# Optimization experiments

Hardware: AMD Instinct MI355X
Metric: run time of the kernel (lower is better)

## Reference

```python
import jax, jax.numpy as jnp
import numpy as np

BN_EPS = 1e-5


def setup_inputs() -> dict:
    key = jax.random.key(0)
    ks = jax.random.split(key, 6)
    B, C, H, W, Lt, Hd = 4, 256, 64, 64, 4096, 128
    w_scale = 1.0 / np.sqrt(C)
    return {
        "input_i": jax.random.normal(ks[0], (B, C, H, W), jnp.float32),
        "input_t": jax.random.normal(ks[1], (B, C, Lt), jnp.float32),
        "w_img_q": jax.random.normal(ks[2], (Hd, C), jnp.float32) * w_scale,
        "bnq_gamma": jnp.ones((Hd,), jnp.float32),
        "bnq_beta": jnp.zeros((Hd,), jnp.float32),
        "bnq_mean": jnp.zeros((Hd,), jnp.float32),
        "bnq_var": jnp.ones((Hd,), jnp.float32),
        "w_img_k": jax.random.normal(ks[3], (Hd, C), jnp.float32) * w_scale,
        "bnk_gamma": jnp.ones((Hd,), jnp.float32),
        "bnk_beta": jnp.zeros((Hd,), jnp.float32),
        "bnk_mean": jnp.zeros((Hd,), jnp.float32),
        "bnk_var": jnp.ones((Hd,), jnp.float32),
        "w_text_k": jax.random.normal(ks[4], (Hd, C), jnp.float32) * w_scale,
        "b_text_k": jnp.zeros((Hd,), jnp.float32),
        "w_text_q": jax.random.normal(ks[5], (Hd, C), jnp.float32) * w_scale,
        "b_text_q": jnp.zeros((Hd,), jnp.float32),
    }


def _conv1x1_bn(x, w, gamma, beta, mean, var):
    # x: [B,C,H,W], w: [O,C] -> [B,O,H,W], then eval-mode BatchNorm2d
    y = jnp.einsum('bchw,oc->bohw', x, w)
    s = (gamma / jnp.sqrt(var + BN_EPS))[None, :, None, None]
    return (y - mean[None, :, None, None]) * s + beta[None, :, None, None]


def reference(input_i, input_t, w_img_q, bnq_gamma, bnq_beta, bnq_mean, bnq_var,
              w_img_k, bnk_gamma, bnk_beta, bnk_mean, bnk_var,
              w_text_k, b_text_k, w_text_q, b_text_q):
    B, C, H, W = input_i.shape
    Hd = w_img_q.shape[0]
    inv_scale = jnp.asarray(Hd, input_i.dtype) ** 0.5  # module divides by hid_dim**-0.5

    # Image -> text attention
    i_q = _conv1x1_bn(input_i, w_img_q, bnq_gamma, bnq_beta, bnq_mean, bnq_var)
    i_q = i_q.reshape(B, Hd, -1).transpose(0, 2, 1)          # [B, Ni, Hd]
    t_flat = input_t.reshape(B, C, -1).transpose(0, 2, 1)    # [B, Lt, C]
    t_k = t_flat @ w_text_k.T + b_text_k                     # [B, Lt, Hd]
    iscores = jnp.einsum('bnd,bmd->bnm', i_q, t_k) * inv_scale
    att_i = jax.nn.softmax(iscores, axis=-1)
    output_i = jnp.einsum('bnm,bmc->bnc', att_i, t_flat)     # [B, Ni, C]

    # Text -> image attention (the permute/reshape/permute chain is identity)
    t_q = t_flat @ w_text_q.T + b_text_q                     # [B, Lt, Hd]
    i_k = _conv1x1_bn(input_i, w_img_k, bnk_gamma, bnk_beta, bnk_mean, bnk_var)
    i_k = i_k.reshape(B, Hd, -1).transpose(0, 2, 1)          # [B, Ni, Hd]
    i_v = input_i.reshape(B, C, -1).transpose(0, 2, 1)       # [B, Ni, C]
    tscores = jnp.einsum('bmd,bnd->bmn', t_q, i_k) * inv_scale
    att_t = jax.nn.softmax(tscores, axis=-1)
    output_t = jnp.einsum('bmn,bnc->bmc', att_t, i_v)        # [B, Lt, C]

    return (output_i, output_t)
```

## Files before the change

### kernel.cpp

```cpp
#include <hip/hip_runtime.h>
#include <hip/hip_bf16.h>
#include <math.h>
#include <stdint.h>

#define B_  4
#define C_  256
#define N_  4096
#define HD_ 128

typedef __attribute__((ext_vector_type(8))) short bf16x8;
typedef __attribute__((ext_vector_type(4))) float f32x4;
typedef __attribute__((ext_vector_type(4))) int   i32x4;

#define WF_SHORTS   ((size_t)4*8*8*2*512)
#define PROJ_SHORTS ((size_t)4*256*4*2*512)
#define VT_SHORTS   ((size_t)4*128*16*512)

static __device__ __forceinline__ short f2bf(float x){
  union { float f; unsigned u; } v; v.f = x;
  unsigned r = v.u + 0x7fffu + ((v.u >> 16) & 1u);
  return (short)(r >> 16);
}
static __device__ __forceinline__ float bf2f(short h){
  union { unsigned u; float f; } v; v.u = ((unsigned)(unsigned short)h) << 16;
  return v.f;
}

__global__ void wfrag_kernel(const float* __restrict__ w0, const float* __restrict__ w1,
                             const float* __restrict__ w2, const float* __restrict__ w3,
                             short* __restrict__ wf)
{
  int job = blockIdx.x, dt = blockIdx.y, ck = blockIdx.z;
  const float* W = job==0 ? w0 : (job==1 ? w1 : (job==2 ? w2 : w3));
  int l = threadIdx.x, g = l>>4, ln = l&15;
  bf16x8 hi, lo;
#pragma unroll
  for (int j=0;j<8;j++){
    int d = dt*16 + ln;
    int c = ck*32 + 4*g + (j&3) + 16*(j>>2);
    float x = W[d*C_ + c];
    short h = f2bf(x);
    hi[j] = h;
    lo[j] = f2bf(x - bf2f(h));
  }
  size_t base = (((size_t)(job*8+dt)*8 + ck)*2)*512 + (size_t)l*8;
  *reinterpret_cast<bf16x8*>(wf + base)       = hi;
  *reinterpret_cast<bf16x8*>(wf + base + 512) = lo;
}

__global__ __launch_bounds__(256,2) void proj_kernel(
    const float* __restrict__ Xi, const float* __restrict__ Xt,
    const short* __restrict__ wf,
    const float* __restrict__ bnq_g, const float* __restrict__ bnq_b,
    const float* __restrict__ bnq_m, const float* __restrict__ bnq_v,
    const float* __restrict__ bnk_g, const float* __restrict__ bnk_b,
    const float* __restrict__ bnk_m, const float* __restrict__ bnk_v,
    const float* __restrict__ btk, const float* __restrict__ btq,
    short* __restrict__ proj)
{
  const int job = blockIdx.z, b = blockIdx.y;
  const int tid = threadIdx.x, wid = tid>>6, l = tid&63, g = l>>4, ln = l&15;
  const float* X = (job==0 || job==3) ? Xi : Xt;
  const int n0 = blockIdx.x*256 + wid*64;

  const f32x4 fzero = {0.f,0.f,0.f,0.f};
  f32x4 acc[4][8];
#pragma unroll
  for (int nt=0;nt<4;nt++)
#pragma unroll
    for (int dt=0;dt<8;dt++) acc[nt][dt] = fzero;

#pragma unroll 1
  for (int ck=0; ck<8; ck++){
    bf16x8 Bh[4], Bl[4];
#pragma unroll
    for (int nt=0;nt<4;nt++){
#pragma unroll
      for (int j=0;j<8;j++){
        int c = ck*32 + 4*g + (j&3) + 16*(j>>2);
        int n = n0 + nt*16 + ln;
        float x = X[((size_t)b*C_ + c)*N_ + n];
        short h = f2bf(x);
        Bh[nt][j] = h;
        Bl[nt][j] = f2bf(x - bf2f(h));
      }
    }
#pragma unroll
    for (int dt=0;dt<8;dt++){
      const short* af = wf + (((size_t)(job*8+dt)*8 + ck)*2)*512 + (size_t)l*8;
      bf16x8 Ah = *reinterpret_cast<const bf16x8*>(af);
      bf16x8 Al = *reinterpret_cast<const bf16x8*>(af + 512);
#pragma unroll
      for (int nt=0;nt<4;nt++){
        acc[nt][dt] = __builtin_amdgcn_mfma_f32_16x16x32_bf16(Ah, Bh[nt], acc[nt][dt], 0,0,0);
        acc[nt][dt] = __builtin_amdgcn_mfma_f32_16x16x32_bf16(Ah, Bl[nt], acc[nt][dt], 0,0,0);
        acc[nt][dt] = __builtin_amdgcn_mfma_f32_16x16x32_bf16(Al, Bh[nt], acc[nt][dt], 0,0,0);
      }
    }
  }

#pragma unroll
  for (int nt=0;nt<4;nt++){
    int tglob = (n0>>4) + nt;
#pragma unroll
    for (int kc=0;kc<4;kc++){
      bf16x8 hi, lo;
#pragma unroll
      for (int j=0;j<8;j++){
        int dt = 2*kc + (j>>2), r = j&3;
        int d = dt*16 + 4*g + r;
        float y = acc[nt][dt][r];
        float s, t;
        if (job==0){ s = bnq_g[d]*rsqrtf(bnq_v[d]+1e-5f); t = bnq_b[d]-bnq_m[d]*s; }
        else if (job==3){ s = bnk_g[d]*rsqrtf(bnk_v[d]+1e-5f); t = bnk_b[d]-bnk_m[d]*s; }
        else if (job==1){ s = 1.f; t = btk[d]; }
        else            { s = 1.f; t = btq[d]; }
        y = y*s + t;
        short h = f2bf(y);
        hi[j] = h;
        lo[j] = f2bf(y - bf2f(h));
      }
      short* dst = proj + (size_t)job*PROJ_SHORTS
                 + ((((size_t)b*256 + tglob)*4 + kc)*2)*512 + (size_t)l*8;
      *reinterpret_cast<bf16x8*>(dst)       = hi;
      *reinterpret_cast<bf16x8*>(dst + 512) = lo;
    }
  }
}

__global__ __launch_bounds__(512,1) void vtile_kernel(
    const float* __restrict__ Xi, const float* __restrict__ Xt,
    short* __restrict__ vt)
{
  int kt = blockIdx.x, b = blockIdx.y, dir = blockIdx.z;
  const float* X = (dir==0) ? Xt : Xi;
  __shared__ float tile[256*33];
  int tid = threadIdx.x;
#pragma unroll
  for (int i=0;i<16;i++){
    int idx = tid + i*512, row = idx>>5, col = idx&31;
    tile[row*33+col] = X[((size_t)b*C_ + row)*N_ + (size_t)kt*32 + col];
  }
  __syncthreads();
  int wid = tid>>6, l = tid&63, g = l>>4, ln = l&15;
#pragma unroll
  for (int w2=0;w2<2;w2++){
    int cc = wid*2 + w2;
    bf16x8 o;
#pragma unroll
    for (int j=0;j<8;j++){
      int c = cc*16 + ln;
      int col = 4*g + (j&3) + 16*(j>>2);
      o[j] = f2bf(tile[c*33 + col]);
    }
    *reinterpret_cast<bf16x8*>(vt + (size_t)dir*VT_SHORTS
        + (((size_t)b*128 + kt)*16 + cc)*512 + (size_t)l*8) = o;
  }
}

__global__ __launch_bounds__(512,2) void flash_kernel(
    const short* __restrict__ proj, const short* __restrict__ vt,
    float* __restrict__ outp)
{
  const int qb = blockIdx.x, b = blockIdx.y, dir = blockIdx.z;
  const short* Qt = proj + (size_t)(2*dir)*PROJ_SHORTS;
  const short* Kt = proj + (size_t)(2*dir+1)*PROJ_SHORTS;
  const short* Vt = vt + (size_t)dir*VT_SHORTS;
  float* Od = outp + (size_t)dir*((size_t)B_*N_*C_);

  __shared__ short lds[2*16384];

  const int tid = threadIdx.x, wid = tid>>6, l = tid&63, g = l>>4, ln = l&15;

  const int tq = qb*8 + wid;
  bf16x8 qf[4][2];
#pragma unroll
  for (int kc=0;kc<4;kc++)
#pragma unroll
    for (int h=0;h<2;h++)
      qf[kc][h] = *reinterpret_cast<const bf16x8*>(
        Qt + ((((size_t)b*256 + tq)*4 + kc)*2 + h)*512 + (size_t)l*8);

  const f32x4 fzero = {0.f,0.f,0.f,0.f};
  f32x4 oacc[16];
#pragma unroll
  for (int cc=0;cc<16;cc++) oacc[cc] = fzero;
  float mrun = -INFINITY, lrun = 0.f;
  const float SCALE = 11.313708498984761f;

  {
    const i32x4* ks = reinterpret_cast<const i32x4*>(Kt + ((size_t)(b*256))*4096) + tid*2;
    const i32x4* vs = reinterpret_cast<const i32x4*>(Vt + ((size_t)(b*128))*8192) + tid*2;
    i32x4 a0=ks[0], a1=ks[1], a2=vs[0], a3=vs[1];
    i32x4* lk = reinterpret_cast<i32x4*>(lds) + tid*2;
    i32x4* lv = reinterpret_cast<i32x4*>(lds + 8192) + tid*2;
    lk[0]=a0; lk[1]=a1; lv[0]=a2; lv[1]=a3;
  }
  __syncthreads();

#pragma unroll 1
  for (int s=0; s<128; s++){
    const int cur = s & 1;
    i32x4 st0, st1, st2, st3;
    if (s < 127){
      const i32x4* ks = reinterpret_cast<const i32x4*>(Kt + ((size_t)(b*256 + 2*(s+1)))*4096) + tid*2;
      const i32x4* vs = reinterpret_cast<const i32x4*>(Vt + ((size_t)(b*128 + (s+1)))*8192) + tid*2;
      st0=ks[0]; st1=ks[1]; st2=vs[0]; st3=vs[1];
    }
    const short* lk = lds + cur*16384;
    const short* lv = lk + 8192;

    f32x4 sacc[2];
    sacc[0] = fzero; sacc[1] = fzero;
#pragma unroll
    for (int kvt=0;kvt<2;kvt++){
#pragma unroll
      for (int kc=0;kc<4;kc++){
        bf16x8 kh  = *reinterpret_cast<const bf16x8*>(lk + (size_t)(kvt*8 + kc*2 + 0)*512 + l*8);
        bf16x8 klo = *reinterpret_cast<const bf16x8*>(lk + (size_t)(kvt*8 + kc*2 + 1)*512 + l*8);
        sacc[kvt] = __builtin_amdgcn_mfma_f32_16x16x32_bf16(kh,  qf[kc][0], sacc[kvt], 0,0,0);
        sacc[kvt] = __builtin_amdgcn_mfma_f32_16x16x32_bf16(kh,  qf[kc][1], sacc[kvt], 0,0,0);
        sacc[kvt] = __builtin_amdgcn_mfma_f32_16x16x32_bf16(klo, qf[kc][0], sacc[kvt], 0,0,0);
      }
    }

    float sv[8];
#pragma unroll
    for (int kvt=0;kvt<2;kvt++)
#pragma unroll
      for (int r=0;r<4;r++) sv[kvt*4+r] = sacc[kvt][r]*SCALE;
    float tmax = sv[0];
#pragma unroll
    for (int i=1;i<8;i++) tmax = fmaxf(tmax, sv[i]);
    tmax = fmaxf(tmax, __shfl_xor(tmax, 16));
    tmax = fmaxf(tmax, __shfl_xor(tmax, 32));
    float mnew  = fmaxf(mrun, tmax);
    float alpha = __expf(mrun - mnew);
    float p[8], psum = 0.f;
#pragma unroll
    for (int i=0;i<8;i++){ p[i] = __expf(sv[i]-mnew); psum += p[i]; }
    psum += __shfl_xor(psum, 16);
    psum += __shfl_xor(psum, 32);
    lrun = lrun*alpha + psum;
    mrun = mnew;

    bf16x8 pa;
#pragma unroll
    for (int i=0;i<8;i++) pa[i] = f2bf(p[i]);
#pragma unroll
    for (int cc=0;cc<16;cc++) oacc[cc] *= alpha;

#pragma unroll
    for (int cc=0;cc<16;cc++){
      bf16x8 vf = *reinterpret_cast<const bf16x8*>(lv + (size_t)cc*512 + l*8);
      oacc[cc] = __builtin_amdgcn_mfma_f32_16x16x32_bf16(vf, pa, oacc[cc], 0,0,0);
    }

    if (s < 127){
      const int nxt = cur^1;
      i32x4* lkw = reinterpret_cast<i32x4*>(lds + nxt*16384) + tid*2;
      i32x4* lvw = reinterpret_cast<i32x4*>(lds + nxt*16384 + 8192) + tid*2;
      lkw[0]=st0; lkw[1]=st1; lvw[0]=st2; lvw[1]=st3;
    }
    __syncthreads();
  }

  float inv = 1.f / lrun;
  int qrow = qb*128 + wid*16 + ln;
  float* orow = Od + ((size_t)b*N_ + qrow)*C_;
#pragma unroll
  for (int cc=0;cc<16;cc++){
    f32x4 o = oacc[cc]*inv;
    *reinterpret_cast<f32x4*>(orow + cc*16 + 4*g) = o;
  }
}

extern "C" void kernel_launch(void* const* d_in, const int* in_sizes, int n_in,
                              void* d_out, int out_size, void* d_ws, size_t ws_size,
                              hipStream_t stream)
{
  (void)in_sizes; (void)n_in; (void)out_size; (void)ws_size;
  const float* input_i = (const float*)d_in[0];
  const float* input_t = (const float*)d_in[1];
  const float* w_img_q = (const float*)d_in[2];
  const float* bnq_g   = (const float*)d_in[3];
  const float* bnq_b   = (const float*)d_in[4];
  const float* bnq_m   = (const float*)d_in[5];
  const float* bnq_v   = (const float*)d_in[6];
  const float* w_img_k = (const float*)d_in[7];
  const float* bnk_g   = (const float*)d_in[8];
  const float* bnk_b   = (const float*)d_in[9];
  const float* bnk_m   = (const float*)d_in[10];
  const float* bnk_v   = (const float*)d_in[11];
  const float* w_text_k = (const float*)d_in[12];
  const float* b_text_k = (const float*)d_in[13];
  const float* w_text_q = (const float*)d_in[14];
  const float* b_text_q = (const float*)d_in[15];

  short* ws   = (short*)d_ws;
  short* wf   = ws;
  short* proj = ws + WF_SHORTS;
  short* vt   = ws + WF_SHORTS + 4*PROJ_SHORTS;

  wfrag_kernel<<<dim3(4,8,8), 64, 0, stream>>>(w_img_q, w_text_k, w_text_q, w_img_k, wf);
  proj_kernel<<<dim3(16,4,4), 256, 0, stream>>>(input_i, input_t, wf,
      bnq_g, bnq_b, bnq_m, bnq_v, bnk_g, bnk_b, bnk_m, bnk_v,
      b_text_k, b_text_q, proj);
  vtile_kernel<<<dim3(128,4,2), 512, 0, stream>>>(input_i, input_t, vt);
  flash_kernel<<<dim3(32,4,2), 512, 0, stream>>>(proj, vt, (float*)d_out);
}
```

Before: 272.5 us.

## Process two query tiles per wave, fold scale into Q, lazy softmax rescale

Each wave now handles two 16-row query tiles, halving the block to 256 threads, so every K and V fragment read from LDS feeds twice as many MFMAs. The softmax scale is folded into the Q projection epilogue, which removes a per-score multiply in the flash loop. The running max is only updated, and the accumulators rescaled, when the new tile max exceeds the old one by more than 8. This trades higher register pressure and fewer waves per CU for less LDS traffic and less per-iteration softmax work.

```diff
diff --git a/kernel.cpp b/kernel.cpp
--- a/kernel.cpp
+++ b/kernel.cpp
@@ -62,6 +62,7 @@
   const int tid = threadIdx.x, wid = tid>>6, l = tid&63, g = l>>4, ln = l&15;
   const float* X = (job==0 || job==3) ? Xi : Xt;
   const int n0 = blockIdx.x*256 + wid*64;
+  const float SCALE = 11.313708498984761f;
 
   const f32x4 fzero = {0.f,0.f,0.f,0.f};
   f32x4 acc[4][8];
@@ -111,10 +112,11 @@
         int d = dt*16 + 4*g + r;
         float y = acc[nt][dt][r];
         float s, t;
-        if (job==0){ s = bnq_g[d]*rsqrtf(bnq_v[d]+1e-5f); t = bnq_b[d]-bnq_m[d]*s; }
+        if (job==0){ s = bnq_g[d]*rsqrtf(bnq_v[d]+1e-5f); t = bnq_b[d]-bnq_m[d]*s;
+                     s *= SCALE; t *= SCALE; }
         else if (job==3){ s = bnk_g[d]*rsqrtf(bnk_v[d]+1e-5f); t = bnk_b[d]-bnk_m[d]*s; }
         else if (job==1){ s = 1.f; t = btk[d]; }
-        else            { s = 1.f; t = btq[d]; }
+        else            { s = SCALE; t = btq[d]*SCALE; }
         y = y*s + t;
         short h = f2bf(y);
         hi[j] = h;
@@ -158,7 +160,7 @@
   }
 }
 
-__global__ __launch_bounds__(512,2) void flash_kernel(
+__global__ __launch_bounds__(256,1) void flash_kernel(
     const short* __restrict__ proj, const short* __restrict__ vt,
     float* __restrict__ outp)
 {
@@ -172,106 +174,132 @@
 
   const int tid = threadIdx.x, wid = tid>>6, l = tid&63, g = l>>4, ln = l&15;
 
-  const int tq = qb*8 + wid;
-  bf16x8 qf[4][2];
-#pragma unroll
-  for (int kc=0;kc<4;kc++)
-#pragma unroll
-    for (int h=0;h<2;h++)
-      qf[kc][h] = *reinterpret_cast<const bf16x8*>(
-        Qt + ((((size_t)b*256 + tq)*4 + kc)*2 + h)*512 + (size_t)l*8);
+  bf16x8 qf[2][4][2];
+#pragma unroll
+  for (int qt=0;qt<2;qt++){
+    const int tq = qb*8 + wid*2 + qt;
+#pragma unroll
+    for (int kc=0;kc<4;kc++)
+#pragma unroll
+      for (int h=0;h<2;h++)
+        qf[qt][kc][h] = *reinterpret_cast<const bf16x8*>(
+          Qt + ((((size_t)b*256 + tq)*4 + kc)*2 + h)*512 + (size_t)l*8);
+  }
 
   const f32x4 fzero = {0.f,0.f,0.f,0.f};
-  f32x4 oacc[16];
-#pragma unroll
-  for (int cc=0;cc<16;cc++) oacc[cc] = fzero;
-  float mrun = -INFINITY, lrun = 0.f;
-  const float SCALE = 11.313708498984761f;
+  f32x4 oacc[2][16];
+#pragma unroll
+  for (int qt=0;qt<2;qt++)
+#pragma unroll
+    for (int cc=0;cc<16;cc++) oacc[qt][cc] = fzero;
+  float mrun[2] = {-INFINITY, -INFINITY};
+  float lrun[2] = {0.f, 0.f};
 
   {
-    const i32x4* ks = reinterpret_cast<const i32x4*>(Kt + ((size_t)(b*256))*4096) + tid*2;
-    const i32x4* vs = reinterpret_cast<const i32x4*>(Vt + ((size_t)(b*128))*8192) + tid*2;
-    i32x4 a0=ks[0], a1=ks[1], a2=vs[0], a3=vs[1];
-    i32x4* lk = reinterpret_cast<i32x4*>(lds) + tid*2;
-    i32x4* lv = reinterpret_cast<i32x4*>(lds + 8192) + tid*2;
-    lk[0]=a0; lk[1]=a1; lv[0]=a2; lv[1]=a3;
+    const i32x4* gk = reinterpret_cast<const i32x4*>(Kt + ((size_t)(b*256))*4096);
+    const i32x4* gv = reinterpret_cast<const i32x4*>(Vt + ((size_t)(b*128))*8192);
+    i32x4* lkw = reinterpret_cast<i32x4*>(lds);
+    i32x4* lvw = reinterpret_cast<i32x4*>(lds + 8192);
+#pragma unroll
+    for (int i=0;i<4;i++){
+      lkw[tid + 256*i] = gk[tid + 256*i];
+      lvw[tid + 256*i] = gv[tid + 256*i];
+    }
   }
   __syncthreads();
 
 #pragma unroll 1
   for (int s=0; s<128; s++){
     const int cur = s & 1;
-    i32x4 st0, st1, st2, st3;
+    i32x4 kst[4], vst[4];
     if (s < 127){
-      const i32x4* ks = reinterpret_cast<const i32x4*>(Kt + ((size_t)(b*256 + 2*(s+1)))*4096) + tid*2;
-      const i32x4* vs = reinterpret_cast<const i32x4*>(Vt + ((size_t)(b*128 + (s+1)))*8192) + tid*2;
-      st0=ks[0]; st1=ks[1]; st2=vs[0]; st3=vs[1];
+      const i32x4* gk = reinterpret_cast<const i32x4*>(Kt + ((size_t)(b*256 + 2*(s+1)))*4096);
+      const i32x4* gv = reinterpret_cast<const i32x4*>(Vt + ((size_t)(b*128 + (s+1)))*8192);
+#pragma unroll
+      for (int i=0;i<4;i++){ kst[i] = gk[tid + 256*i]; vst[i] = gv[tid + 256*i]; }
     }
     const short* lk = lds + cur*16384;
     const short* lv = lk + 8192;
 
-    f32x4 sacc[2];
-    sacc[0] = fzero; sacc[1] = fzero;
+    f32x4 sacc[2][2];
+    sacc[0][0]=fzero; sacc[0][1]=fzero; sacc[1][0]=fzero; sacc[1][1]=fzero;
 #pragma unroll
     for (int kvt=0;kvt<2;kvt++){
 #pragma unroll
       for (int kc=0;kc<4;kc++){
         bf16x8 kh  = *reinterpret_cast<const bf16x8*>(lk + (size_t)(kvt*8 + kc*2 + 0)*512 + l*8);
         bf16x8 klo = *reinterpret_cast<const bf16x8*>(lk + (size_t)(kvt*8 + kc*2 + 1)*512 + l*8);
-        sacc[kvt] = __builtin_amdgcn_mfma_f32_16x16x32_bf16(kh,  qf[kc][0], sacc[kvt], 0,0,0);
-        sacc[kvt] = __builtin_amdgcn_mfma_f32_16x16x32_bf16(kh,  qf[kc][1], sacc[kvt], 0,0,0);
-        sacc[kvt] = __builtin_amdgcn_mfma_f32_16x16x32_bf16(klo, qf[kc][0], sacc[kvt], 0,0,0);
-      }
-    }
-
-    float sv[8];
-#pragma unroll
-    for (int kvt=0;kvt<2;kvt++)
-#pragma unroll
-      for (int r=0;r<4;r++) sv[kvt*4+r] = sacc[kvt][r]*SCALE;
-    float tmax = sv[0];
-#pragma unroll
-    for (int i=1;i<8;i++) tmax = fmaxf(tmax, sv[i]);
-    tmax = fmaxf(tmax, __shfl_xor(tmax, 16));
-    tmax = fmaxf(tmax, __shfl_xor(tmax, 32));
-    float mnew  = fmaxf(mrun, tmax);
-    float alpha = __expf(mrun - mnew);
-    float p[8], psum = 0.f;
-#pragma unroll
-    for (int i=0;i<8;i++){ p[i] = __expf(sv[i]-mnew); psum += p[i]; }
-    psum += __shfl_xor(psum, 16);
-    psum += __shfl_xor(psum, 32);
-    lrun = lrun*alpha + psum;
-    mrun = mnew;
-
-    bf16x8 pa;
-#pragma unroll
-    for (int i=0;i<8;i++) pa[i] = f2bf(p[i]);
-#pragma unroll
-    for (int cc=0;cc<16;cc++) oacc[cc] *= alpha;
+#pragma unroll
+        for (int qt=0;qt<2;qt++){
+          sacc[qt][kvt] = __builtin_amdgcn_mfma_f32_16x16x32_bf16(kh,  qf[qt][kc][0], sacc[qt][kvt], 0,0,0);
+          sacc[qt][kvt] = __builtin_amdgcn_mfma_f32_16x16x32_bf16(kh,  qf[qt][kc][1], sacc[qt][kvt], 0,0,0);
+          sacc[qt][kvt] = __builtin_amdgcn_mfma_f32_16x16x32_bf16(klo, qf[qt][kc][0], sacc[qt][kvt], 0,0,0);
+        }
+      }
+    }
+
+    bf16x8 pa[2];
+#pragma unroll
+    for (int qt=0;qt<2;qt++){
+      float sv[8];
+#pragma unroll
+      for (int kvt=0;kvt<2;kvt++)
+#pragma unroll
+        for (int r=0;r<4;r++) sv[kvt*4+r] = sacc[qt][kvt][r];
+      float tmax = sv[0];
+#pragma unroll
+      for (int i=1;i<8;i++) tmax = fmaxf(tmax, sv[i]);
+      tmax = fmaxf(tmax, __shfl_xor(tmax, 16));
+      tmax = fmaxf(tmax, __shfl_xor(tmax, 32));
+      if (__all(tmax - mrun[qt] <= 8.f)){
+        float psum = 0.f;
+#pragma unroll
+        for (int i=0;i<8;i++){ float p = __expf(sv[i]-mrun[qt]); pa[qt][i] = f2bf(p); psum += p; }
+        psum += __shfl_xor(psum, 16);
+        psum += __shfl_xor(psum, 32);
+        lrun[qt] += psum;
+      } else {
+        float mnew  = fmaxf(mrun[qt], tmax);
+        float alpha = __expf(mrun[qt] - mnew);
+        float psum = 0.f;
+#pragma unroll
+        for (int i=0;i<8;i++){ float p = __expf(sv[i]-mnew); pa[qt][i] = f2bf(p); psum += p; }
+        psum += __shfl_xor(psum, 16);
+        psum += __shfl_xor(psum, 32);
+        lrun[qt] = lrun[qt]*alpha + psum;
+        mrun[qt] = mnew;
+#pragma unroll
+        for (int cc=0;cc<16;cc++) oacc[qt][cc] *= alpha;
+      }
+    }
 
 #pragma unroll
     for (int cc=0;cc<16;cc++){
       bf16x8 vf = *reinterpret_cast<const bf16x8*>(lv + (size_t)cc*512 + l*8);
-      oacc[cc] = __builtin_amdgcn_mfma_f32_16x16x32_bf16(vf, pa, oacc[cc], 0,0,0);
+      oacc[0][cc] = __builtin_amdgcn_mfma_f32_16x16x32_bf16(vf, pa[0], oacc[0][cc], 0,0,0);
+      oacc[1][cc] = __builtin_amdgcn_mfma_f32_16x16x32_bf16(vf, pa[1], oacc[1][cc], 0,0,0);
     }
 
     if (s < 127){
       const int nxt = cur^1;
-      i32x4* lkw = reinterpret_cast<i32x4*>(lds + nxt*16384) + tid*2;
-      i32x4* lvw = reinterpret_cast<i32x4*>(lds + nxt*16384 + 8192) + tid*2;
-      lkw[0]=st0; lkw[1]=st1; lvw[0]=st2; lvw[1]=st3;
+      i32x4* lkw = reinterpret_cast<i32x4*>(lds + nxt*16384);
+      i32x4* lvw = reinterpret_cast<i32x4*>(lds + nxt*16384 + 8192);
+#pragma unroll
+      for (int i=0;i<4;i++){ lkw[tid + 256*i] = kst[i]; lvw[tid + 256*i] = vst[i]; }
     }
     __syncthreads();
   }
 
-  float inv = 1.f / lrun;
-  int qrow = qb*128 + wid*16 + ln;
-  float* orow = Od + ((size_t)b*N_ + qrow)*C_;
-#pragma unroll
-  for (int cc=0;cc<16;cc++){
-    f32x4 o = oacc[cc]*inv;
-    *reinterpret_cast<f32x4*>(orow + cc*16 + 4*g) = o;
+#pragma unroll
+  for (int qt=0;qt<2;qt++){
+    float inv = 1.f / lrun[qt];
+    int qrow = (qb*8 + wid*2 + qt)*16 + ln;
+    float* orow = Od + ((size_t)b*N_ + qrow)*C_;
+#pragma unroll
+    for (int cc=0;cc<16;cc++){
+      f32x4 o = oacc[qt][cc]*inv;
+      *reinterpret_cast<f32x4*>(orow + cc*16 + 4*g) = o;
+    }
   }
 }
 
@@ -307,5 +335,5 @@
       bnq_g, bnq_b, bnq_m, bnq_v, bnk_g, bnk_b, bnk_m, bnk_v,
       b_text_k, b_text_q, proj);
   vtile_kernel<<<dim3(128,4,2), 512, 0, stream>>>(input_i, input_t, vt);
-  flash_kernel<<<dim3(32,4,2), 512, 0, stream>>>(proj, vt, (float*)d_out);
-}
+  flash_kernel<<<dim3(32,4,2), 256, 0, stream>>>(proj, vt, (float*)d_out);
+}
```

New measurement: 387.7 us. 42.3% more time.

## Fold softmax scale into Q projection, lazy rescale, coalesced LDS staging, setprio

Applied to the files above, without the earlier changes.

Moves the attention scale factor into the Q projection epilogue so the flash loop no longer multiplies scores. Adds a lazy online-softmax rescale that skips the max update and output rescaling when the new max exceeds the running max by at most 8 across the wave. Changes K/V staging to coalesced strided indexing and wraps the MFMA blocks in s_setprio to favour matrix issue. The lazy rescale lets exponentials reach up to e^8 before renormalising, a small risk for bf16 precision of P.

```diff
diff --git a/kernel.cpp b/kernel.cpp
--- a/kernel.cpp
+++ b/kernel.cpp
@@ -62,6 +62,7 @@
   const int tid = threadIdx.x, wid = tid>>6, l = tid&63, g = l>>4, ln = l&15;
   const float* X = (job==0 || job==3) ? Xi : Xt;
   const int n0 = blockIdx.x*256 + wid*64;
+  const float SCALE = 11.313708498984761f;
 
   const f32x4 fzero = {0.f,0.f,0.f,0.f};
   f32x4 acc[4][8];
@@ -111,10 +112,11 @@
         int d = dt*16 + 4*g + r;
         float y = acc[nt][dt][r];
         float s, t;
-        if (job==0){ s = bnq_g[d]*rsqrtf(bnq_v[d]+1e-5f); t = bnq_b[d]-bnq_m[d]*s; }
+        if (job==0){ s = bnq_g[d]*rsqrtf(bnq_v[d]+1e-5f); t = bnq_b[d]-bnq_m[d]*s;
+                     s *= SCALE; t *= SCALE; }
         else if (job==3){ s = bnk_g[d]*rsqrtf(bnk_v[d]+1e-5f); t = bnk_b[d]-bnk_m[d]*s; }
         else if (job==1){ s = 1.f; t = btk[d]; }
-        else            { s = 1.f; t = btq[d]; }
+        else            { s = SCALE; t = btq[d]*SCALE; }
         y = y*s + t;
         short h = f2bf(y);
         hi[j] = h;
@@ -186,32 +188,33 @@
 #pragma unroll
   for (int cc=0;cc<16;cc++) oacc[cc] = fzero;
   float mrun = -INFINITY, lrun = 0.f;
-  const float SCALE = 11.313708498984761f;
 
   {
-    const i32x4* ks = reinterpret_cast<const i32x4*>(Kt + ((size_t)(b*256))*4096) + tid*2;
-    const i32x4* vs = reinterpret_cast<const i32x4*>(Vt + ((size_t)(b*128))*8192) + tid*2;
-    i32x4 a0=ks[0], a1=ks[1], a2=vs[0], a3=vs[1];
-    i32x4* lk = reinterpret_cast<i32x4*>(lds) + tid*2;
-    i32x4* lv = reinterpret_cast<i32x4*>(lds + 8192) + tid*2;
-    lk[0]=a0; lk[1]=a1; lv[0]=a2; lv[1]=a3;
+    const i32x4* gk = reinterpret_cast<const i32x4*>(Kt + ((size_t)(b*256))*4096);
+    const i32x4* gv = reinterpret_cast<const i32x4*>(Vt + ((size_t)(b*128))*8192);
+    i32x4* lkw = reinterpret_cast<i32x4*>(lds);
+    i32x4* lvw = reinterpret_cast<i32x4*>(lds + 8192);
+#pragma unroll
+    for (int i=0;i<2;i++){ lkw[tid+512*i] = gk[tid+512*i]; lvw[tid+512*i] = gv[tid+512*i]; }
   }
   __syncthreads();
 
 #pragma unroll 1
   for (int s=0; s<128; s++){
     const int cur = s & 1;
-    i32x4 st0, st1, st2, st3;
+    i32x4 kst[2], vst[2];
     if (s < 127){
-      const i32x4* ks = reinterpret_cast<const i32x4*>(Kt + ((size_t)(b*256 + 2*(s+1)))*4096) + tid*2;
-      const i32x4* vs = reinterpret_cast<const i32x4*>(Vt + ((size_t)(b*128 + (s+1)))*8192) + tid*2;
-      st0=ks[0]; st1=ks[1]; st2=vs[0]; st3=vs[1];
+      const i32x4* gk = reinterpret_cast<const i32x4*>(Kt + ((size_t)(b*256 + 2*(s+1)))*4096);
+      const i32x4* gv = reinterpret_cast<const i32x4*>(Vt + ((size_t)(b*128 + (s+1)))*8192);
+#pragma unroll
+      for (int i=0;i<2;i++){ kst[i] = gk[tid+512*i]; vst[i] = gv[tid+512*i]; }
     }
     const short* lk = lds + cur*16384;
     const short* lv = lk + 8192;
 
     f32x4 sacc[2];
     sacc[0] = fzero; sacc[1] = fzero;
+    __builtin_amdgcn_s_setprio(1);
 #pragma unroll
     for (int kvt=0;kvt<2;kvt++){
 #pragma unroll
@@ -223,44 +226,52 @@
         sacc[kvt] = __builtin_amdgcn_mfma_f32_16x16x32_bf16(klo, qf[kc][0], sacc[kvt], 0,0,0);
       }
     }
+    __builtin_amdgcn_s_setprio(0);
 
     float sv[8];
 #pragma unroll
     for (int kvt=0;kvt<2;kvt++)
 #pragma unroll
-      for (int r=0;r<4;r++) sv[kvt*4+r] = sacc[kvt][r]*SCALE;
+      for (int r=0;r<4;r++) sv[kvt*4+r] = sacc[kvt][r];
     float tmax = sv[0];
 #pragma unroll
     for (int i=1;i<8;i++) tmax = fmaxf(tmax, sv[i]);
     tmax = fmaxf(tmax, __shfl_xor(tmax, 16));
     tmax = fmaxf(tmax, __shfl_xor(tmax, 32));
-    float mnew  = fmaxf(mrun, tmax);
-    float alpha = __expf(mrun - mnew);
-    float p[8], psum = 0.f;
-#pragma unroll
-    for (int i=0;i<8;i++){ p[i] = __expf(sv[i]-mnew); psum += p[i]; }
+
+    bf16x8 pa;
+    float psum = 0.f;
+    if (__all(tmax - mrun <= 8.f)){
+#pragma unroll
+      for (int i=0;i<8;i++){ float p = __expf(sv[i]-mrun); pa[i] = f2bf(p); psum += p; }
+    } else {
+      float mnew  = fmaxf(mrun, tmax);
+      float alpha = __expf(mrun - mnew);
+#pragma unroll
+      for (int i=0;i<8;i++){ float p = __expf(sv[i]-mnew); pa[i] = f2bf(p); psum += p; }
+      lrun *= alpha;
+      mrun = mnew;
+#pragma unroll
+      for (int cc=0;cc<16;cc++) oacc[cc] *= alpha;
+    }
     psum += __shfl_xor(psum, 16);
     psum += __shfl_xor(psum, 32);
-    lrun = lrun*alpha + psum;
-    mrun = mnew;
-
-    bf16x8 pa;
-#pragma unroll
-    for (int i=0;i<8;i++) pa[i] = f2bf(p[i]);
-#pragma unroll
-    for (int cc=0;cc<16;cc++) oacc[cc] *= alpha;
-
+    lrun += psum;
+
+    __builtin_amdgcn_s_setprio(1);
 #pragma unroll
     for (int cc=0;cc<16;cc++){
       bf16x8 vf = *reinterpret_cast<const bf16x8*>(lv + (size_t)cc*512 + l*8);
       oacc[cc] = __builtin_amdgcn_mfma_f32_16x16x32_bf16(vf, pa, oacc[cc], 0,0,0);
     }
+    __builtin_amdgcn_s_setprio(0);
 
     if (s < 127){
       const int nxt = cur^1;
-      i32x4* lkw = reinterpret_cast<i32x4*>(lds + nxt*16384) + tid*2;
-      i32x4* lvw = reinterpret_cast<i32x4*>(lds + nxt*16384 + 8192) + tid*2;
-      lkw[0]=st0; lkw[1]=st1; lvw[0]=st2; lvw[1]=st3;
+      i32x4* lkw = reinterpret_cast<i32x4*>(lds + nxt*16384);
+      i32x4* lvw = reinterpret_cast<i32x4*>(lds + nxt*16384 + 8192);
+#pragma unroll
+      for (int i=0;i<2;i++){ lkw[tid+512*i] = kst[i]; lvw[tid+512*i] = vst[i]; }
     }
     __syncthreads();
   }
@@ -300,12 +311,12 @@
   short* ws   = (short*)d_ws;
   short* wf   = ws;
   short* proj = ws + WF_SHORTS;
-  short* vt   = ws + WF_SHORTS + 4*PROJ_SHORTS;
+  short* vtb  = ws + WF_SHORTS + 4*PROJ_SHORTS;
 
   wfrag_kernel<<<dim3(4,8,8), 64, 0, stream>>>(w_img_q, w_text_k, w_text_q, w_img_k, wf);
   proj_kernel<<<dim3(16,4,4), 256, 0, stream>>>(input_i, input_t, wf,
       bnq_g, bnq_b, bnq_m, bnq_v, bnk_g, bnk_b, bnk_m, bnk_v,
       b_text_k, b_text_q, proj);
-  vtile_kernel<<<dim3(128,4,2), 512, 0, stream>>>(input_i, input_t, vt);
-  flash_kernel<<<dim3(32,4,2), 512, 0, stream>>>(proj, vt, (float*)d_out);
-}
+  vtile_kernel<<<dim3(128,4,2), 512, 0, stream>>>(input_i, input_t, vtb);
+  flash_kernel<<<dim3(32,4,2), 512, 0, stream>>>(proj, vtb, (float*)d_out);
+}
```

New measurement: 274.5 us. No clear change (+0.8%).
